# Kernel optimization log

Measured on AMD Instinct MI355X. Metric: run time of the kernel, lower is better.

Reference implementation:

```python
import jax, jax.numpy as jnp
import numpy as np

N, S, M, Y = 64, 64, 32, 1000
RANKS = [64, 128, 256, 512, 512, 512]  # len == log2(N)
B = 4096


def setup_inputs() -> dict:
    key = jax.random.key(0)
    ks = jax.random.split(key, 20)
    rn = lambda k, shape, fan: jax.random.normal(k, shape, dtype=jnp.float32) / np.float32(np.sqrt(fan))
    inp = {}
    inp["X"] = jax.random.normal(ks[0], (B, N, S), dtype=jnp.float32)
    # repr MLP: s->128->64->32->M (torch Linear stored here as (in,out))
    inp["W1"], inp["b1"] = rn(ks[1], (S, 128), S), jnp.zeros((128,), jnp.float32)
    inp["W2"], inp["b2"] = rn(ks[2], (128, 64), 128), jnp.zeros((64,), jnp.float32)
    inp["W3"], inp["b3"] = rn(ks[3], (64, 32), 64), jnp.zeros((32,), jnp.float32)
    inp["W4"], inp["b4"] = rn(ks[4], (32, M), 32), jnp.zeros((M,), jnp.float32)
    # HT tree parameters (scaled randn for numerical stability through 6 levels)
    inp["P0"] = rn(ks[5], (N, RANKS[0], M), M)                 # leaves
    L = len(RANKS)
    for l in range(1, L):
        inp[f"P{l}"] = rn(ks[5 + l], (N // 2 ** l, RANKS[l], RANKS[l - 1]), RANKS[l - 1])
    inp["Ptop"] = rn(ks[5 + L], (Y, RANKS[-1]), RANKS[-1])
    return inp


def reference(X, W1, b1, W2, b2, W3, b3, W4, b4, P0, P1, P2, P3, P4, P5, Ptop):
    # representation MLP: (B, N, s) -> (B, N, M)
    h = jax.nn.relu(X @ W1 + b1)
    h = jax.nn.relu(h @ W2 + b2)
    h = jax.nn.relu(h @ W3 + b3)
    F = h @ W4 + b4  # (B, N, M)
    # Leaf contraction: t[b,j,a] = sum_m P0[j,a,m] * F[b,j,m]
    t = jnp.einsum("jam,bjm->bja", P0, F)  # (B, N, r0)
    # Bottom-up HT tree contraction. Equivalent to the nested kron construction:
    # t_l[b,j,g] = sum_a P_l[j,g,a] * t_{l-1}[b,2j,a] * t_{l-1}[b,2j+1,a]
    for P in (P1, P2, P3, P4, P5):
        prod = t[:, 0::2] * t[:, 1::2]          # (B, n/2, r_prev)
        t = jnp.einsum("jga,bja->bjg", P, prod)  # (B, n/2, r_l)
    pair = t[:, 0] * t[:, 1]                     # (B, r_last)
    # h[b,y] = sum_a Ptop[y,a] * pair[b,a]  == sum(A[y] * rank-1 factor)
    return pair @ Ptop.T  # (B, Y)
```

## Files before the change

### kernel.cpp

```cpp
#include <hip/hip_runtime.h>


typedef short short8 __attribute__((ext_vector_type(8)));
typedef float floatx16 __attribute__((ext_vector_type(16)));

__device__ __forceinline__ unsigned bf16_rne(float x) {
    unsigned u = __float_as_uint(x);
    return (u + 0x7FFFu + ((u >> 16) & 1u)) >> 16;
}
__device__ __forceinline__ float bf16_f(unsigned h) { return __uint_as_float(h << 16); }
__device__ __forceinline__ void split2(float x, unsigned& h, unsigned& m) {
    h = bf16_rne(x);
    float r = x - bf16_f(h);
    m = bf16_rne(r);
}

struct Seg { const float* src; long dst; int Z, G, Gpad, K, trans, blk0; };
struct SegTable { Seg s[11]; };

__global__ __launch_bounds__(256) void presplit(SegTable T, unsigned short* P) {
    int blk = blockIdx.x;
    int si = 0;
#pragma unroll
    for (int i = 1; i < 11; ++i) if (blk >= T.s[i].blk0) si = i;
    Seg d = T.s[si];
    const int K8 = d.K >> 3;
    long total = (long)d.Z * d.Gpad * K8;
    long o = (long)(blk - d.blk0) * 256 + threadIdx.x;
    if (o >= total) return;
    int k8 = (int)(o % K8);
    long rem = o / K8;
    int g = (int)(rem % d.Gpad);
    int z = (int)(rem / d.Gpad);
    float e[8];
    if (g < d.G) {
        if (!d.trans) {
            const float* s = d.src + ((long)z * d.G + g) * d.K + k8 * 8;
            float4 a = *(const float4*)s, b = *(const float4*)(s + 4);
            e[0]=a.x; e[1]=a.y; e[2]=a.z; e[3]=a.w; e[4]=b.x; e[5]=b.y; e[6]=b.z; e[7]=b.w;
        } else {
#pragma unroll
            for (int i = 0; i < 8; ++i) e[i] = d.src[(long)(k8 * 8 + i) * d.G + g];
        }
    } else {
#pragma unroll
        for (int i = 0; i < 8; ++i) e[i] = 0.f;
    }
    unsigned h[8], m[8];
#pragma unroll
    for (int i = 0; i < 8; ++i) split2(e[i], h[i], m[i]);
    uint4 Ph = { h[0]|(h[1]<<16), h[2]|(h[3]<<16), h[4]|(h[5]<<16), h[6]|(h[7]<<16) };
    uint4 Pm = { m[0]|(m[1]<<16), m[2]|(m[3]<<16), m[4]|(m[5]<<16), m[6]|(m[7]<<16) };
    const int NGTt = d.Gpad >> 5;
    const int KC16 = d.K >> 4;
    const long slot = (long)((g & 31) | ((k8 & 1) << 5)) * 8;
    long fh = ((long)(z * 2 + 0) * KC16 + (k8 >> 1)) * NGTt + (g >> 5);
    long fm = ((long)(z * 2 + 1) * KC16 + (k8 >> 1)) * NGTt + (g >> 5);
    *(uint4*)&P[d.dst + fh * 512 + slot] = Ph;
    *(uint4*)&P[d.dst + fm * 512 + slot] = Pm;
}

template<int BT, int GTW, int GWAVES, int MINW, int PAIR>
__global__ __launch_bounds__(256, MINW) void ht_mfma(
    const float* __restrict__ Act,
    const unsigned short* __restrict__ Wp,
    const float* __restrict__ bias,
    float* __restrict__ C,
    int K, int Gtot, int NGTtot,
    long act_z, long act_pair, int act_rb,
    long c_z, int c_rb, int relu)
{
    constexpr int BWAVES = 4 / GWAVES;
    constexpr int BB  = BWAVES * BT * 32;
    constexpr int GG  = GWAVES * GTW * 32;
    constexpr int NBT = BB / 32;
    constexpr int NR  = BB / 64;

    __shared__ unsigned short AS[2 * NBT * 1024];

    const int tid  = threadIdx.x;
    const int lane = tid & 63;
    const int w    = tid >> 6;
    const int bw   = w % BWAVES;
    const int gw   = w / BWAVES;

    const int b0  = blockIdx.x * BB;
    const int g0t = blockIdx.y * (GG / 32);
    const int g0  = blockIdx.y * GG;
    const int z   = blockIdx.z;

    const float* Abase = Act + (long)z * act_z + (long)b0 * act_rb;
    const int aslot = ((lane & 31) * 2 + (lane >> 5)) * 8;
    const unsigned short* Wl = Wp + lane * 8;
    const int KC16 = K >> 4;

    auto stage = [&](int k0) {
#pragma unroll
        for (int r = 0; r < NR; ++r) {
            const int s = r * 256 + tid;
            const int b = s >> 2, oct = s & 3;
            const float* p = Abase + (long)b * act_rb + k0 + oct * 8;
            float4 v0 = *(const float4*)p;
            float4 v1 = *(const float4*)(p + 4);
            if (PAIR) {
                float4 u0 = *(const float4*)(p + act_pair);
                float4 u1 = *(const float4*)(p + act_pair + 4);
                v0.x *= u0.x; v0.y *= u0.y; v0.z *= u0.z; v0.w *= u0.w;
                v1.x *= u1.x; v1.y *= u1.y; v1.z *= u1.z; v1.w *= u1.w;
            }
            float e[8] = { v0.x, v0.y, v0.z, v0.w, v1.x, v1.y, v1.z, v1.w };
            unsigned h[8], m[8];
#pragma unroll
            for (int i = 0; i < 8; ++i) split2(e[i], h[i], m[i]);
            uint4 Ph = { h[0]|(h[1]<<16), h[2]|(h[3]<<16), h[4]|(h[5]<<16), h[6]|(h[7]<<16) };
            uint4 Pm = { m[0]|(m[1]<<16), m[2]|(m[3]<<16), m[4]|(m[5]<<16), m[6]|(m[7]<<16) };
            const int base = (b >> 5) * 1024 + (oct >> 1) * 512 + ((b & 31) * 2 + (oct & 1)) * 8;
            *(uint4*)&AS[base] = Ph;
            *(uint4*)&AS[NBT * 1024 + base] = Pm;
        }
    };

    floatx16 acc[BT][GTW];
#pragma unroll
    for (int bt = 0; bt < BT; ++bt)
#pragma unroll
        for (int gt = 0; gt < GTW; ++gt) acc[bt][gt] = (floatx16)0.f;

    stage(0);
    __syncthreads();

    for (int k0 = 0; k0 < K; k0 += 32) {
#pragma unroll
        for (int kc = 0; kc < 2; ++kc) {
            short8 wf[2][GTW];
#pragma unroll
            for (int sa = 0; sa < 2; ++sa)
#pragma unroll
                for (int gt = 0; gt < GTW; ++gt) {
                    const long frag = ((long)(z * 2 + sa) * KC16 + (k0 >> 4) + kc) * NGTtot
                                      + g0t + gw * GTW + gt;
                    wf[sa][gt] = *(const short8*)(Wl + frag * 512);
                }
            short8 af[2][BT];
#pragma unroll
            for (int sb = 0; sb < 2; ++sb)
#pragma unroll
                for (int bt = 0; bt < BT; ++bt)
                    af[sb][bt] = *(const short8*)&AS[(sb * NBT + bw * BT + bt) * 1024
                                                     + kc * 512 + aslot];
#pragma unroll
            for (int gt = 0; gt < GTW; ++gt) {
#pragma unroll
                for (int bt = 0; bt < BT; ++bt)
                    acc[bt][gt] = __builtin_amdgcn_mfma_f32_32x32x16_bf16(
                        wf[0][gt], af[0][bt], acc[bt][gt], 0, 0, 0);
#pragma unroll
                for (int bt = 0; bt < BT; ++bt)
                    acc[bt][gt] = __builtin_amdgcn_mfma_f32_32x32x16_bf16(
                        wf[0][gt], af[1][bt], acc[bt][gt], 0, 0, 0);
#pragma unroll
                for (int bt = 0; bt < BT; ++bt)
                    acc[bt][gt] = __builtin_amdgcn_mfma_f32_32x32x16_bf16(
                        wf[1][gt], af[0][bt], acc[bt][gt], 0, 0, 0);
            }
        }
        if (k0 + 32 < K) {
            __syncthreads();
            stage(k0 + 32);
            __syncthreads();
        }
    }

    const int koct = lane >> 5;
#pragma unroll
    for (int bt = 0; bt < BT; ++bt) {
        const int b = b0 + bw * (BT * 32) + bt * 32 + (lane & 31);
        float* crow = C + (long)z * c_z + (long)b * c_rb;
#pragma unroll
        for (int gt = 0; gt < GTW; ++gt) {
            const int gb = g0 + gw * (GTW * 32) + gt * 32 + 4 * koct;
#pragma unroll
            for (int r4 = 0; r4 < 4; ++r4) {
                const int g = gb + r4 * 8;
                float4 o;
                o.x = acc[bt][gt][r4 * 4 + 0];
                o.y = acc[bt][gt][r4 * 4 + 1];
                o.z = acc[bt][gt][r4 * 4 + 2];
                o.w = acc[bt][gt][r4 * 4 + 3];
                if (bias) {
                    float4 bv = *(const float4*)(bias + g);
                    o.x += bv.x; o.y += bv.y; o.z += bv.z; o.w += bv.w;
                }
                if (relu) {
                    o.x = fmaxf(o.x, 0.f); o.y = fmaxf(o.y, 0.f);
                    o.z = fmaxf(o.z, 0.f); o.w = fmaxf(o.w, 0.f);
                }
                if (g + 3 < Gtot) {
                    *(float4*)(crow + g) = o;
                } else if (g < Gtot) {
                    crow[g] = o.x;
                    if (g + 1 < Gtot) crow[g + 1] = o.y;
                    if (g + 2 < Gtot) crow[g + 2] = o.z;
                }
            }
        }
    }
}

extern "C" void kernel_launch(void* const* d_in, const int* in_sizes, int n_in,
                              void* d_out, int out_size, void* d_ws, size_t ws_size,
                              hipStream_t stream)
{
    const float* X    = (const float*)d_in[0];
    const float* W1   = (const float*)d_in[1];
    const float* b1   = (const float*)d_in[2];
    const float* W2   = (const float*)d_in[3];
    const float* b2   = (const float*)d_in[4];
    const float* W3   = (const float*)d_in[5];
    const float* b3   = (const float*)d_in[6];
    const float* W4   = (const float*)d_in[7];
    const float* b4   = (const float*)d_in[8];
    const float* P0   = (const float*)d_in[9];
    const float* P1   = (const float*)d_in[10];
    const float* P2   = (const float*)d_in[11];
    const float* P3   = (const float*)d_in[12];
    const float* P4   = (const float*)d_in[13];
    const float* P5   = (const float*)d_in[14];
    const float* Ptop = (const float*)d_in[15];
    float* out = (float*)d_out;

    unsigned short* planes = (unsigned short*)d_ws;
    float* base = (float*)d_ws;
    float* h1c = base + 6291456L;
    float* h2c = base + 23068672L;
    float* h3c = base + 6291456L;
    float* Fc  = base + 10485760L;
    float* t0  = base + 31457280L;
    float* t1  = base + 6291456L;
    float* t2  = base + 23068672L;
    float* t3  = base + 6291456L;
    float* t4  = base + 39845888L;
    float* t5  = base + 23068672L;

    SegTable T;
    auto seg = [](const float* s, long dst, int Z, int G, int Gpad, int K, int tr, int b0) {
        Seg d; d.src=s; d.dst=dst; d.Z=Z; d.G=G; d.Gpad=Gpad; d.K=K; d.trans=tr; d.blk0=b0; return d;
    };
    T.s[0]  = seg(W1,   0L,        1, 128, 128,  64, 1, 0);
    T.s[1]  = seg(W2,   16384L,    1,  64,  64, 128, 1, 4);
    T.s[2]  = seg(W3,   32768L,    1,  32,  32,  64, 1, 8);
    T.s[3]  = seg(W4,   36864L,    1,  32,  32,  32, 1, 9);
    T.s[4]  = seg(P0,   38912L,   64,  64,  64,  32, 0, 10);
    T.s[5]  = seg(P1,   301056L,  32, 128, 128,  64, 0, 74);
    T.s[6]  = seg(P2,   825344L,  16, 256, 256, 128, 0, 202);
    T.s[7]  = seg(P3,   1873920L,  8, 512, 512, 256, 0, 458);
    T.s[8]  = seg(P4,   3971072L,  4, 512, 512, 512, 0, 970);
    T.s[9]  = seg(P5,   6068224L,  2, 512, 512, 512, 0, 1482);
    T.s[10] = seg(Ptop, 7116800L,  1, 1000, 1024, 512, 0, 1738);
    presplit<<<dim3(1994), dim3(256), 0, stream>>>(T, planes);

    dim3 blk(256, 1, 1);

    for (int c = 0; c < 2; ++c) {
        const float* Xc = X + (long)c * 131072 * 64;
        ht_mfma<2, 2, 2, 3, 0><<<dim3(1024, 1, 1), blk, 0, stream>>>(
            Xc, planes + 0, b1, h1c, 64, 128, 4, 0L, 0L, 64, 0L, 128, 1);
        ht_mfma<2, 1, 2, 3, 0><<<dim3(1024, 1, 1), blk, 0, stream>>>(
            h1c, planes + 16384, b2, h2c, 128, 64, 2, 0L, 0L, 128, 0L, 64, 1);
        ht_mfma<2, 1, 1, 3, 0><<<dim3(512, 1, 1), blk, 0, stream>>>(
            h2c, planes + 32768, b3, h3c, 64, 32, 1, 0L, 0L, 64, 0L, 32, 1);
        ht_mfma<2, 1, 1, 3, 0><<<dim3(512, 1, 1), blk, 0, stream>>>(
            h3c, planes + 36864, b4, Fc, 32, 32, 1, 0L, 0L, 32, 0L, 32, 0);
        ht_mfma<2, 1, 2, 3, 0><<<dim3(16, 1, 64), blk, 0, stream>>>(
            Fc, planes + 38912, nullptr, t0 + (long)c * 131072, 32, 64, 2,
            32L, 0L, 2048, 262144L, 64, 0);
    }

    ht_mfma<2, 2, 2, 3, 1><<<dim3(32, 1, 32), blk, 0, stream>>>(
        t0, planes + 301056, nullptr, t1, 64, 128, 4,
        524288L, 262144L, 64, 524288L, 128, 0);
    ht_mfma<2, 4, 2, 2, 1><<<dim3(32, 1, 16), blk, 0, stream>>>(
        t1, planes + 825344, nullptr, t2, 128, 256, 8,
        1048576L, 524288L, 128, 1048576L, 256, 0);
    ht_mfma<2, 4, 2, 2, 1><<<dim3(32, 2, 8), blk, 0, stream>>>(
        t2, planes + 1873920, nullptr, t3, 256, 512, 16,
        2097152L, 1048576L, 256, 2097152L, 512, 0);
    ht_mfma<2, 2, 2, 3, 1><<<dim3(32, 4, 4), blk, 0, stream>>>(
        t3, planes + 3971072, nullptr, t4, 512, 512, 16,
        4194304L, 2097152L, 512, 2097152L, 512, 0);
    ht_mfma<1, 2, 2, 3, 1><<<dim3(64, 4, 2), blk, 0, stream>>>(
        t4, planes + 6068224, nullptr, t5, 512, 512, 16,
        4194304L, 2097152L, 512, 2097152L, 512, 0);
    ht_mfma<1, 2, 2, 3, 1><<<dim3(64, 8, 1), blk, 0, stream>>>(
        t5, planes + 7116800, nullptr, out, 512, 1000, 32,
        0L, 2097152L, 512, 0L, 1000, 0);
}
```

Measured before the change: 512.1 us.

## Fuse representation MLP and leaf contraction into one LDS-resident kernel

Replaces the ten per-chunk launches for the four MLP layers and the leaf contraction with a single kernel. Each block takes 64 batch rows of one leaf j, keeps the split bf16 hi/lo activations in shared memory between layers, and writes only t0 to global memory. This removes the global round-trips of the h1, h2, h3 and F intermediates and the launch overhead. In exchange it uses 64KB of LDS per block, which limits occupancy, and leaves waves idle in the narrow layers.

```diff
diff --git a/kernel.cpp b/kernel.cpp
--- a/kernel.cpp
+++ b/kernel.cpp
@@ -58,6 +58,124 @@
     long fm = ((long)(z * 2 + 1) * KC16 + (k8 >> 1)) * NGTt + (g >> 5);
     *(uint4*)&P[d.dst + fh * 512 + slot] = Ph;
     *(uint4*)&P[d.dst + fm * 512 + slot] = Pm;
+}
+
+__global__ __launch_bounds__(256, 2) void ht_fused(
+    const float* __restrict__ X,
+    const unsigned short* __restrict__ Wpl,
+    const float* __restrict__ b1, const float* __restrict__ b2,
+    const float* __restrict__ b3, const float* __restrict__ b4,
+    float* __restrict__ t0)
+{
+    __shared__ unsigned short AS[32768];
+    const int tid  = threadIdx.x;
+    const int lane = tid & 63, w = tid >> 6;
+    const int bw   = w & 1, gw = w >> 1;
+    const int b31  = lane & 31, koct = lane >> 5;
+    const int aslot = (b31 * 2 + koct) * 8;
+    const int b0 = blockIdx.x * 64;
+    const int j  = blockIdx.y;
+
+#pragma unroll
+    for (int it = 0; it < 2; ++it) {
+        const int s = it * 256 + tid;
+        const int b = s >> 3, k8 = s & 7;
+        const float* p = X + ((long)(b0 + b) * 64 + j) * 64 + k8 * 8;
+        float4 v0 = *(const float4*)p, v1 = *(const float4*)(p + 4);
+        float e[8] = { v0.x, v0.y, v0.z, v0.w, v1.x, v1.y, v1.z, v1.w };
+        unsigned h[8], m[8];
+#pragma unroll
+        for (int i = 0; i < 8; ++i) split2(e[i], h[i], m[i]);
+        uint4 Ph = { h[0]|(h[1]<<16), h[2]|(h[3]<<16), h[4]|(h[5]<<16), h[6]|(h[7]<<16) };
+        uint4 Pm = { m[0]|(m[1]<<16), m[2]|(m[3]<<16), m[4]|(m[5]<<16), m[6]|(m[7]<<16) };
+        const int bt = b >> 3 >> 2;
+        const int slot = ((b & 31) * 2 + (k8 & 1)) * 8;
+        const int kc = k8 >> 1;
+        *(uint4*)&AS[((0 * 2 + bt) * 4 + kc) * 512 + slot] = Ph;
+        *(uint4*)&AS[((1 * 2 + bt) * 4 + kc) * 512 + slot] = Pm;
+    }
+    __syncthreads();
+
+    floatx16 acc[2];
+
+    auto comp = [&](int srcbase, int KC, const unsigned short* Wb, int NGTt,
+                    int gts, int ntg) {
+#pragma unroll
+        for (int gt = 0; gt < 2; ++gt) acc[gt] = (floatx16)0.f;
+        for (int kc = 0; kc < KC; ++kc) {
+            short8 af0 = *(const short8*)&AS[srcbase + ((0 * 2 + bw) * KC + kc) * 512 + aslot];
+            short8 af1 = *(const short8*)&AS[srcbase + ((1 * 2 + bw) * KC + kc) * 512 + aslot];
+#pragma unroll
+            for (int gt = 0; gt < 2; ++gt) {
+                if (gt >= ntg) continue;
+                const unsigned short* f0 = Wb + ((long)(0 * KC + kc) * NGTt + gts + gt) * 512 + lane * 8;
+                const unsigned short* f1 = Wb + ((long)(1 * KC + kc) * NGTt + gts + gt) * 512 + lane * 8;
+                short8 w0 = *(const short8*)f0;
+                short8 w1 = *(const short8*)f1;
+                acc[gt] = __builtin_amdgcn_mfma_f32_32x32x16_bf16(w0, af0, acc[gt], 0, 0, 0);
+                acc[gt] = __builtin_amdgcn_mfma_f32_32x32x16_bf16(w0, af1, acc[gt], 0, 0, 0);
+                acc[gt] = __builtin_amdgcn_mfma_f32_32x32x16_bf16(w1, af0, acc[gt], 0, 0, 0);
+            }
+        }
+    };
+
+    auto wb = [&](int ntg, int gts, const float* bias, int relu,
+                  int dstbase, int KCd) {
+#pragma unroll
+        for (int gt = 0; gt < 2; ++gt) {
+            if (gt >= ntg) continue;
+            const int gtile = gts + gt;
+#pragma unroll
+            for (int gg = 0; gg < 4; ++gg) {
+                float4 bv = make_float4(0.f, 0.f, 0.f, 0.f);
+                if (bias) bv = *(const float4*)(bias + gtile * 32 + gg * 8 + koct * 4);
+                float o[4] = { acc[gt][gg*4+0] + bv.x, acc[gt][gg*4+1] + bv.y,
+                               acc[gt][gg*4+2] + bv.z, acc[gt][gg*4+3] + bv.w };
+                if (relu) {
+#pragma unroll
+                    for (int i = 0; i < 4; ++i) o[i] = fmaxf(o[i], 0.f);
+                }
+                unsigned h[4], m[4];
+#pragma unroll
+                for (int i = 0; i < 4; ++i) split2(o[i], h[i], m[i]);
+                const int kcd  = gtile * 2 + (gg >> 1);
+                const int slot = (b31 * 2 + (gg & 1)) * 8 + koct * 4;
+                uint2 ph = { h[0] | (h[1] << 16), h[2] | (h[3] << 16) };
+                uint2 pm = { m[0] | (m[1] << 16), m[2] | (m[3] << 16) };
+                *(uint2*)&AS[dstbase + ((0 * 2 + bw) * KCd + kcd) * 512 + slot] = ph;
+                *(uint2*)&AS[dstbase + ((1 * 2 + bw) * KCd + kcd) * 512 + slot] = pm;
+            }
+        }
+    };
+
+    comp(0, 4, Wpl + 0, 4, gw * 2, 2);
+    wb(2, gw * 2, b1, 1, 8192, 8);
+    __syncthreads();
+    comp(8192, 8, Wpl + 16384, 2, gw, 1);
+    wb(1, gw, b2, 1, 24576, 4);
+    __syncthreads();
+    if (gw == 0) {
+        comp(24576, 4, Wpl + 32768, 1, 0, 1);
+        wb(1, 0, b3, 1, 0, 2);
+    }
+    __syncthreads();
+    if (gw == 0) {
+        comp(0, 2, Wpl + 36864, 1, 0, 1);
+        wb(1, 0, b4, 0, 4096, 2);
+    }
+    __syncthreads();
+    comp(4096, 2, Wpl + 38912 + (long)j * 4096, 2, gw, 1);
+    {
+        const int bglob = b0 + bw * 32 + b31;
+        float* crow = t0 + (long)j * 262144 + (long)bglob * 64;
+#pragma unroll
+        for (int gg = 0; gg < 4; ++gg) {
+            const int g = gw * 32 + gg * 8 + koct * 4;
+            float4 o = make_float4(acc[0][gg*4+0], acc[0][gg*4+1],
+                                   acc[0][gg*4+2], acc[0][gg*4+3]);
+            *(float4*)(crow + g) = o;
+        }
+    }
 }
 
 template<int BT, int GTW, int GWAVES, int MINW, int PAIR>
@@ -231,10 +349,6 @@
 
     unsigned short* planes = (unsigned short*)d_ws;
     float* base = (float*)d_ws;
-    float* h1c = base + 6291456L;
-    float* h2c = base + 23068672L;
-    float* h3c = base + 6291456L;
-    float* Fc  = base + 10485760L;
     float* t0  = base + 31457280L;
     float* t1  = base + 6291456L;
     float* t2  = base + 23068672L;
@@ -261,20 +375,8 @@
 
     dim3 blk(256, 1, 1);
 
-    for (int c = 0; c < 2; ++c) {
-        const float* Xc = X + (long)c * 131072 * 64;
-        ht_mfma<2, 2, 2, 3, 0><<<dim3(1024, 1, 1), blk, 0, stream>>>(
-            Xc, planes + 0, b1, h1c, 64, 128, 4, 0L, 0L, 64, 0L, 128, 1);
-        ht_mfma<2, 1, 2, 3, 0><<<dim3(1024, 1, 1), blk, 0, stream>>>(
-            h1c, planes + 16384, b2, h2c, 128, 64, 2, 0L, 0L, 128, 0L, 64, 1);
-        ht_mfma<2, 1, 1, 3, 0><<<dim3(512, 1, 1), blk, 0, stream>>>(
-            h2c, planes + 32768, b3, h3c, 64, 32, 1, 0L, 0L, 64, 0L, 32, 1);
-        ht_mfma<2, 1, 1, 3, 0><<<dim3(512, 1, 1), blk, 0, stream>>>(
-            h3c, planes + 36864, b4, Fc, 32, 32, 1, 0L, 0L, 32, 0L, 32, 0);
-        ht_mfma<2, 1, 2, 3, 0><<<dim3(16, 1, 64), blk, 0, stream>>>(
-            Fc, planes + 38912, nullptr, t0 + (long)c * 131072, 32, 64, 2,
-            32L, 0L, 2048, 262144L, 64, 0);
-    }
+    ht_fused<<<dim3(64, 64, 1), blk, 0, stream>>>(
+        X, planes, b1, b2, b3, b4, t0);
 
     ht_mfma<2, 2, 2, 3, 1><<<dim3(32, 1, 32), blk, 0, stream>>>(
         t0, planes + 301056, nullptr, t1, 64, 128, 4,
```

Result: faster. 434.7 us (-15.1%).
